# Kernel tuning notes

Hardware: AMD Instinct MI355X
Metric: run time of the kernel (lower is better)

The kernel has to match this reference:

```python
import jax, jax.numpy as jnp
import numpy as np

EPS = 1e-5
NUM_HEADS = 4

# Spiking neuron: single-timestep LIF with threshold 1.0 (Heaviside forward,
# ATan surrogate gradient as in snntorch's default spike_grad).
@jax.custom_vjp
def spike(v):
    return (v >= 1.0).astype(v.dtype)

def _spike_fwd(v):
    return spike(v), v

def _spike_bwd(v, g):
    u = v - 1.0
    return (g / (1.0 + (jnp.pi * u) ** 2),)

spike.defvjp(_spike_fwd, _spike_bwd)

def layernorm(x, g, b):
    mu = jnp.mean(x, axis=-1, keepdims=True)
    var = jnp.var(x, axis=-1, keepdims=True)
    return (x - mu) * jax.lax.rsqrt(var + EPS) * g + b

def batchnorm(x, g, b):
    # BatchNorm1d applied on (B, C, N) == per-channel stats over (B, N) of (B, N, C)
    mu = jnp.mean(x, axis=(0, 1))
    var = jnp.var(x, axis=(0, 1))
    return (x - mu) * jax.lax.rsqrt(var + EPS) * g + b

def lin_bn_spike(x, w, g, b):
    # Linear (no bias) -> BatchNorm1d -> spiking neuron
    return spike(batchnorm(jnp.einsum('bnc,oc->bno', x, w), g, b))


def setup_inputs() -> dict:
    key = jax.random.key(0)
    ks = jax.random.split(key, 8)
    B, N, C = 8, 2048, 256
    Hid = 1024  # int(256 * 4.0)
    s = 0.02
    d = {
        'x': jax.random.normal(ks[0], (B, N, C), jnp.float32),
        'ln1_g': jnp.ones((C,), jnp.float32), 'ln1_b': jnp.zeros((C,), jnp.float32),
        'wq': jax.random.normal(ks[1], (C, C), jnp.float32) * s,
        'q_g': jnp.ones((C,), jnp.float32), 'q_b': jnp.zeros((C,), jnp.float32),
        'wk': jax.random.normal(ks[2], (C, C), jnp.float32) * s,
        'k_g': jnp.ones((C,), jnp.float32), 'k_b': jnp.zeros((C,), jnp.float32),
        'wv': jax.random.normal(ks[3], (C, C), jnp.float32) * s,
        'v_g': jnp.ones((C,), jnp.float32), 'v_b': jnp.zeros((C,), jnp.float32),
        'wo': jax.random.normal(ks[4], (C, C), jnp.float32) * s,
        'ln2_g': jnp.ones((C,), jnp.float32), 'ln2_b': jnp.zeros((C,), jnp.float32),
        'w1': jax.random.normal(ks[5], (Hid, C), jnp.float32) * s,
        'bn1_g': jnp.ones((Hid,), jnp.float32), 'bn1_b': jnp.zeros((Hid,), jnp.float32),
        'w2': jax.random.normal(ks[6], (C, Hid), jnp.float32) * s,
        'bn2_g': jnp.ones((C,), jnp.float32), 'bn2_b': jnp.zeros((C,), jnp.float32),
    }
    return d


def reference(x, ln1_g, ln1_b, wq, q_g, q_b, wk, k_g, k_b, wv, v_g, v_b, wo,
              ln2_g, ln2_b, w1, bn1_g, bn1_b, w2, bn2_g, bn2_b):
    B, N, C = x.shape
    H = NUM_HEADS
    D = C // H
    scale = D ** (-0.5)

    # --- Spiking self-attention on norm1(x) ---
    h = layernorm(x, ln1_g, ln1_b)
    q = lin_bn_spike(h, wq, q_g, q_b)
    k = lin_bn_spike(h, wk, k_g, k_b)
    v = lin_bn_spike(h, wv, v_g, v_b)
    qh = q.reshape(B, N, H, D).transpose(0, 2, 1, 3)
    kh = k.reshape(B, N, H, D).transpose(0, 2, 1, 3)
    vh = v.reshape(B, N, H, D).transpose(0, 2, 1, 3)
    attn = jnp.einsum('bhnd,bhmd->bhnm', qh, kh) * scale  # no softmax
    o = jnp.einsum('bhnm,bhmd->bhnd', attn, vh)
    o = o.transpose(0, 2, 1, 3).reshape(B, N, C)
    x = x + jnp.einsum('bnc,oc->bno', o, wo)

    # --- Spiking MLP on norm2(x) (dropout=0.0) ---
    h = layernorm(x, ln2_g, ln2_b)
    m = lin_bn_spike(h, w1, bn1_g, bn1_b)
    m = lin_bn_spike(m, w2, bn2_g, bn2_b)
    return x + m
```

## Files before the change

kernel.cpp:

```cpp
#include <hip/hip_runtime.h>
#include <cstddef>
#include <cstdint>

#define RR 16384
#define CC 256
#define NN 2048

typedef __attribute__((ext_vector_type(8))) _Float16 h8;
typedef __attribute__((ext_vector_type(4))) float float4v;
typedef unsigned short u16;

__device__ inline float h2f(u16 u) {
  return (float)__builtin_bit_cast(_Float16, u);
}
__device__ inline u16 f2h(float f) {
  return __builtin_bit_cast(u16, (_Float16)f);
}

__global__ __launch_bounds__(256) void ln_split(const float* __restrict__ x,
    const float* __restrict__ g, const float* __restrict__ b,
    u16* __restrict__ out) {
  const int wave = threadIdx.x >> 6, lane = threadIdx.x & 63;
  const int row = (blockIdx.x << 2) + wave;
  const float4 v = ((const float4*)(x + (size_t)row * CC))[lane];
  float s1 = v.x + v.y + v.z + v.w;
  float s2 = v.x * v.x + v.y * v.y + v.z * v.z + v.w * v.w;
#pragma unroll
  for (int o = 32; o > 0; o >>= 1) {
    s1 += __shfl_xor(s1, o);
    s2 += __shfl_xor(s2, o);
  }
  const float mu = s1 * (1.0f / CC);
  const float var = s2 * (1.0f / CC) - mu * mu;
  const float rs = 1.0f / sqrtf(var + 1e-5f);
  const float4 gg = ((const float4*)g)[lane];
  const float4 bb = ((const float4*)b)[lane];
  float o4[4];
  o4[0] = (v.x - mu) * rs * gg.x + bb.x;
  o4[1] = (v.y - mu) * rs * gg.y + bb.y;
  o4[2] = (v.z - mu) * rs * gg.z + bb.z;
  o4[3] = (v.w - mu) * rs * gg.w + bb.w;
  ushort4 hi, lo;
  hi.x = f2h(o4[0]); lo.x = f2h(o4[0] - h2f(hi.x));
  hi.y = f2h(o4[1]); lo.y = f2h(o4[1] - h2f(hi.y));
  hi.z = f2h(o4[2]); lo.z = f2h(o4[2] - h2f(hi.z));
  hi.w = f2h(o4[3]); lo.w = f2h(o4[3] - h2f(hi.w));
  *(ushort4*)(out + (size_t)row * 512 + (lane << 2)) = hi;
  *(ushort4*)(out + (size_t)row * 512 + 256 + (lane << 2)) = lo;
}

__global__ __launch_bounds__(256) void split_all(const float* __restrict__ wq,
    const float* __restrict__ wk, const float* __restrict__ wv,
    const float* __restrict__ wo, const float* __restrict__ w1,
    const float* __restrict__ w2, u16* __restrict__ Wqkv,
    u16* __restrict__ wo2, u16* __restrict__ w12, u16* __restrict__ w22) {
  const int bid = blockIdx.x;
  if (bid < 768) {
    const float* W = (bid < 256) ? wq : (bid < 512) ? wk : wv;
    const int rowoff = (bid >> 8) << 8;
    const int li = (bid & 255) * 256 + threadIdx.x;
    const int o = li >> 8, k = li & 255;
    const float w = W[li];
    const u16 h1 = f2h(w);
    const u16 h2 = f2h(w - h2f(h1));
    u16* base = Wqkv + (size_t)(o + rowoff) * 768;
    base[k] = h1; base[256 + k] = h1; base[512 + k] = h2;
  } else if (bid < 1024) {
    const int li = (bid - 768) * 256 + threadIdx.x;
    const int o = li >> 8, k = li & 255;
    const float w = wo[li];
    const u16 h1 = f2h(w);
    const u16 h2 = f2h(w - h2f(h1));
    u16* base = wo2 + (size_t)o * 512;
    base[k] = h1; base[256 + k] = h2;
  } else if (bid < 2048) {
    const int li = (bid - 1024) * 256 + threadIdx.x;
    w12[li] = f2h(w1[li]);
  } else {
    const int li = (bid - 2048) * 256 + threadIdx.x;
    w22[li] = f2h(w2[li]);
  }
}

template <int BM, int BN, int WM, int WN, int STATS, int MINW, int OUTF16>
__global__ __launch_bounds__(512, MINW) void gemm_sp(
    const u16* __restrict__ A, int AW,
    const u16* __restrict__ W2, int K2,
    const float* __restrict__ resid, void* __restrict__ Yv, int O,
    float* __restrict__ p1, float* __restrict__ p2) {
  constexpr int FM = BM / (WM * 16);
  constexpr int FN = BN / (WN * 16);
  constexpr int LA = BM / 64;
  constexpr int LB = BN / 64;
  constexpr int NL = LA + LB;
  static_assert(WM * WN == 8, "8 waves");
  static_assert(NL == 3 || NL == 4 || NL == 5 || NL == 7 || NL == 8,
                "vmcnt literal");
  __shared__ __align__(16) u16 As[2][BM * 64];
  __shared__ __align__(16) u16 Bs[2][BN * 64];
  const int tid = threadIdx.x;
  const int lane = tid & 63, wid = tid >> 6;
  const int wr = wid / WN, wc = wid % WN;
  const int gx = gridDim.x;
  const int lid = blockIdx.y * gx + blockIdx.x;
  const int chunk = (gx * gridDim.y) >> 3;
  const int nid = (lid & 7) * chunk + (lid >> 3);
  const int bx = nid % gx, by = nid / gx;
  const int r0 = by * BM, o0 = bx * BN;
  const int lrow = tid >> 3;
  const int lce = ((tid & 7) ^ ((tid >> 3) & 7)) << 3;

  auto STAGE = [&](int buf, int kAs, int k0s) {
#pragma unroll
    for (int i = 0; i < LA; ++i) {
      const u16* srcA = A + (size_t)(r0 + i * 64 + lrow) * AW + kAs + lce;
      __builtin_amdgcn_global_load_lds(
          (const __attribute__((address_space(1))) void*)srcA,
          (__attribute__((address_space(3))) void*)&As[buf][(i * 64 + wid * 8) * 64],
          16, 0, 0);
    }
#pragma unroll
    for (int i = 0; i < LB; ++i) {
      const u16* srcB = W2 + (size_t)(o0 + i * 64 + lrow) * K2 + k0s + lce;
      __builtin_amdgcn_global_load_lds(
          (const __attribute__((address_space(1))) void*)srcB,
          (__attribute__((address_space(3))) void*)&Bs[buf][(i * 64 + wid * 8) * 64],
          16, 0, 0);
    }
  };

  float4v acc[FM][FN] = {};
  STAGE(0, 0, 0);
  int kA = 0, cur = 0;
  for (int k0 = 0; k0 < K2; k0 += 64) {
    const int kAn = (kA + 64) & (AW - 1);
    if (k0 + 64 < K2) {
      STAGE(cur ^ 1, kAn, k0 + 64);
      if constexpr (NL == 3)
        asm volatile("s_waitcnt vmcnt(3)\n\ts_barrier" ::: "memory");
      else if constexpr (NL == 4)
        asm volatile("s_waitcnt vmcnt(4)\n\ts_barrier" ::: "memory");
      else if constexpr (NL == 5)
        asm volatile("s_waitcnt vmcnt(5)\n\ts_barrier" ::: "memory");
      else if constexpr (NL == 7)
        asm volatile("s_waitcnt vmcnt(7)\n\ts_barrier" ::: "memory");
      else
        asm volatile("s_waitcnt vmcnt(8)\n\ts_barrier" ::: "memory");
    } else {
      asm volatile("s_waitcnt vmcnt(0)\n\ts_barrier" ::: "memory");
    }
#pragma unroll
    for (int kk = 0; kk < 2; ++kk) {
      h8 a[FM], b[FN];
      const int ch0 = (kk << 2) + (lane >> 4);
      const int chs = ch0 ^ (lane & 7);
#pragma unroll
      for (int m = 0; m < FM; ++m) {
        const int R = wr * (FM * 16) + m * 16 + (lane & 15);
        a[m] = *(const h8*)&As[cur][R * 64 + chs * 8];
      }
#pragma unroll
      for (int n = 0; n < FN; ++n) {
        const int Rb = wc * (FN * 16) + n * 16 + (lane & 15);
        b[n] = *(const h8*)&Bs[cur][Rb * 64 + chs * 8];
      }
#pragma unroll
      for (int m = 0; m < FM; ++m)
#pragma unroll
        for (int n = 0; n < FN; ++n)
          acc[m][n] = __builtin_amdgcn_mfma_f32_16x16x32_f16(a[m], b[n], acc[m][n], 0, 0, 0);
    }
    asm volatile("s_waitcnt lgkmcnt(0)\n\ts_barrier" ::: "memory");
    kA = kAn; cur ^= 1;
  }
  const int crow = (lane >> 4) << 2, ccol = lane & 15;
#pragma unroll
  for (int m = 0; m < FM; ++m)
#pragma unroll
    for (int n = 0; n < FN; ++n)
#pragma unroll
      for (int j = 0; j < 4; ++j) {
        const size_t idx =
            (size_t)(r0 + wr * (FM * 16) + (m << 4) + crow + j) * O +
            o0 + wc * (FN * 16) + (n << 4) + ccol;
        float v = acc[m][n][j];
        if constexpr (OUTF16) {
          ((u16*)Yv)[idx] = f2h(v);
        } else {
          if (resid) v += resid[idx];
          ((float*)Yv)[idx] = v;
        }
      }
  if (STATS) {
    float s1[FN], s2[FN];
#pragma unroll
    for (int n = 0; n < FN; ++n) {
      s1[n] = 0.f; s2[n] = 0.f;
#pragma unroll
      for (int m = 0; m < FM; ++m)
#pragma unroll
        for (int j = 0; j < 4; ++j) {
          const float v = acc[m][n][j];
          s1[n] += v; s2[n] += v * v;
        }
    }
#pragma unroll
    for (int n = 0; n < FN; ++n) {
      s1[n] += __shfl_xor(s1[n], 16); s1[n] += __shfl_xor(s1[n], 32);
      s2[n] += __shfl_xor(s2[n], 16); s2[n] += __shfl_xor(s2[n], 32);
    }
    float* sb = (float*)As;
    __syncthreads();
    if (lane < 16) {
#pragma unroll
      for (int n = 0; n < FN; ++n) {
        const int cl = wc * (FN * 16) + n * 16 + lane;
        sb[wr * BN + cl] = s1[n];
        sb[WM * BN + wr * BN + cl] = s2[n];
      }
    }
    __syncthreads();
    if (tid < BN) {
      float a = 0.f, b = 0.f;
#pragma unroll
      for (int w = 0; w < WM; ++w) {
        a += sb[w * BN + tid];
        b += sb[WM * BN + w * BN + tid];
      }
      p1[(size_t)by * O + o0 + tid] = a;
      p2[(size_t)by * O + o0 + tid] = b;
    }
  }
}

__global__ __launch_bounds__(256) void bn_stats2(const float* __restrict__ p1,
    const float* __restrict__ p2, float* __restrict__ mu,
    float* __restrict__ rinv, int O, int npanels) {
  const int c0 = blockIdx.x << 6;
  const int c = threadIdx.x & 63;
  const int jg = threadIdx.x >> 6;
  float s1 = 0.f, s2 = 0.f;
#pragma unroll 4
  for (int j = jg; j < npanels; j += 4) {
    s1 += p1[(size_t)j * O + c0 + c];
    s2 += p2[(size_t)j * O + c0 + c];
  }
  __shared__ float sb[8][64];
  sb[jg][c] = s1;
  sb[4 + jg][c] = s2;
  __syncthreads();
  if (threadIdx.x < 64) {
    const float a = ((sb[0][c] + sb[1][c]) + (sb[2][c] + sb[3][c]));
    const float b = ((sb[4][c] + sb[5][c]) + (sb[6][c] + sb[7][c]));
    const float m = a * (1.0f / 16384.f);
    const float v = b * (1.0f / 16384.f) - m * m;
    mu[c0 + c] = m;
    rinv[c0 + c] = 1.0f / sqrtf(v + 1e-5f);
  }
}

__global__ __launch_bounds__(256) void bn_spike_h16(const u16* __restrict__ Y,
    const float* __restrict__ mu, const float* __restrict__ rinv,
    const float* __restrict__ g, const float* __restrict__ b,
    u16* __restrict__ S, int O) {
  const int i = blockIdx.x * 256 + threadIdx.x;
  const int c = (i << 2) & (O - 1);
  const ushort4 yh = ((const ushort4*)Y)[i];
  const float4 m4 = *(const float4*)(mu + c);
  const float4 r4 = *(const float4*)(rinv + c);
  const float4 g4 = *(const float4*)(g + c);
  const float4 b4 = *(const float4*)(b + c);
  ushort4 s;
  s.x = ((h2f(yh.x) - m4.x) * r4.x * g4.x + b4.x >= 1.0f) ? (u16)0x3C00 : (u16)0;
  s.y = ((h2f(yh.y) - m4.y) * r4.y * g4.y + b4.y >= 1.0f) ? (u16)0x3C00 : (u16)0;
  s.z = ((h2f(yh.z) - m4.z) * r4.z * g4.z + b4.z >= 1.0f) ? (u16)0x3C00 : (u16)0;
  s.w = ((h2f(yh.w) - m4.w) * r4.w * g4.w + b4.w >= 1.0f) ? (u16)0x3C00 : (u16)0;
  ((ushort4*)S)[i] = s;
}

__global__ __launch_bounds__(256) void bn_spike_add(const float* __restrict__ Y,
    const float* __restrict__ mu, const float* __restrict__ rinv,
    const float* __restrict__ g, const float* __restrict__ b,
    float* __restrict__ addOut, int O) {
  const int i = blockIdx.x * 256 + threadIdx.x;
  const int c = (i << 2) & (O - 1);
  const float4 y = ((const float4*)Y)[i];
  const float4 m4 = *(const float4*)(mu + c);
  const float4 r4 = *(const float4*)(rinv + c);
  const float4 g4 = *(const float4*)(g + c);
  const float4 b4 = *(const float4*)(b + c);
  float4 o4 = ((const float4*)addOut)[i];
  o4.x += ((y.x - m4.x) * r4.x * g4.x + b4.x >= 1.0f) ? 1.0f : 0.0f;
  o4.y += ((y.y - m4.y) * r4.y * g4.y + b4.y >= 1.0f) ? 1.0f : 0.0f;
  o4.z += ((y.z - m4.z) * r4.z * g4.z + b4.z >= 1.0f) ? 1.0f : 0.0f;
  o4.w += ((y.w - m4.w) * r4.w * g4.w + b4.w >= 1.0f) ? 1.0f : 0.0f;
  ((float4*)addOut)[i] = o4;
}

__global__ __launch_bounds__(256) void attn_kv(const float* __restrict__ Yq,
    const float* __restrict__ mu, const float* __restrict__ rinv,
    const float* __restrict__ kg, const float* __restrict__ kb,
    const float* __restrict__ vg, const float* __restrict__ vb,
    float* __restrict__ Mpart) {
  const int bh = blockIdx.x, sp = blockIdx.y;
  const int b = bh >> 2, h = bh & 3;
  const int t = threadIdx.x;
  const int gq = t >> 6, e = t & 63;
  __shared__ float ks[16][64], vs[16][64];
  float acc[16] = {};
  const int lrow = t >> 4, lf = (t & 15) << 2;
  const int c = (h << 6) + lf;
  const int ck = 256 + c, cv = 512 + c;
  const float4 kmu = *(const float4*)(mu + ck);
  const float4 krv = *(const float4*)(rinv + ck);
  const float4 kg4 = *(const float4*)(kg + c);
  const float4 kb4 = *(const float4*)(kb + c);
  const float4 vmu = *(const float4*)(mu + cv);
  const float4 vrv = *(const float4*)(rinv + cv);
  const float4 vg4 = *(const float4*)(vg + c);
  const float4 vb4 = *(const float4*)(vb + c);
  for (int n0 = sp * 128; n0 < sp * 128 + 128; n0 += 16) {
    const size_t rowb = (size_t)(b * NN + n0 + lrow) * 768;
    const float4 kq = *(const float4*)(Yq + rowb + ck);
    const float4 vq = *(const float4*)(Yq + rowb + cv);
    __syncthreads();
    ks[lrow][lf + 0] = ((kq.x - kmu.x) * krv.x * kg4.x + kb4.x >= 1.0f) ? 1.f : 0.f;
    ks[lrow][lf + 1] = ((kq.y - kmu.y) * krv.y * kg4.y + kb4.y >= 1.0f) ? 1.f : 0.f;
    ks[lrow][lf + 2] = ((kq.z - kmu.z) * krv.z * kg4.z + kb4.z >= 1.0f) ? 1.f : 0.f;
    ks[lrow][lf + 3] = ((kq.w - kmu.w) * krv.w * kg4.w + kb4.w >= 1.0f) ? 1.f : 0.f;
    vs[lrow][lf + 0] = ((vq.x - vmu.x) * vrv.x * vg4.x + vb4.x >= 1.0f) ? 1.f : 0.f;
    vs[lrow][lf + 1] = ((vq.y - vmu.y) * vrv.y * vg4.y + vb4.y >= 1.0f) ? 1.f : 0.f;
    vs[lrow][lf + 2] = ((vq.z - vmu.z) * vrv.z * vg4.z + vb4.z >= 1.0f) ? 1.f : 0.f;
    vs[lrow][lf + 3] = ((vq.w - vmu.w) * vrv.w * vg4.w + vb4.w >= 1.0f) ? 1.f : 0.f;
    __syncthreads();
#pragma unroll
    for (int nn = 0; nn < 16; ++nn) {
      const float vv = vs[nn][e];
#pragma unroll
      for (int i = 0; i < 16; ++i) acc[i] += ks[nn][(gq << 4) + i] * vv;
    }
  }
  float* mp = Mpart + ((size_t)bh * 16 + sp) * 4096;
#pragma unroll
  for (int i = 0; i < 16; ++i) mp[((gq << 4) + i) * 64 + e] = acc[i];
}

__global__ __launch_bounds__(256) void attn_kv_reduce(
    const float* __restrict__ Mpart, float* __restrict__ M) {
  const int i = blockIdx.x * 256 + threadIdx.x;
  const int bh = i >> 12, j = i & 4095;
  float s = 0.f;
#pragma unroll
  for (int sp = 0; sp < 16; ++sp)
    s += Mpart[((size_t)bh * 16 + sp) * 4096 + j];
  M[i] = s;
}

__global__ __launch_bounds__(256) void attn_qm(const float* __restrict__ Yq,
    const float* __restrict__ mu, const float* __restrict__ rinv,
    const float* __restrict__ qg, const float* __restrict__ qb,
    const float* __restrict__ M, u16* __restrict__ O2) {
  const int h = blockIdx.x;
  const int r0 = blockIdx.y << 6;
  const int b = blockIdx.y >> 5;
  const int t = threadIdx.x;
  const int e = t & 63, rg = t >> 6;
  __shared__ float Ms[64][64];
  __shared__ float qs[64][64];
  const float* Mb = M + ((size_t)(b * 4 + h) << 12);
  for (int i = t; i < 4096; i += 256) ((float*)Ms)[i] = Mb[i];
  const int c = (h << 6) + e;
  const float qmu = mu[c], qrv = rinv[c], qgg = qg[c], qbb = qb[c];
  for (int rl = rg; rl < 64; rl += 4) {
    const float y = Yq[(size_t)(r0 + rl) * 768 + c];
    qs[rl][e] = ((y - qmu) * qrv * qgg + qbb >= 1.0f) ? 1.f : 0.f;
  }
  __syncthreads();
  for (int rl = rg; rl < 64; rl += 4) {
    float acc = 0.f;
#pragma unroll
    for (int d = 0; d < 64; ++d) acc += qs[rl][d] * Ms[d][e];
    const float o = 0.125f * acc;
    const u16 hi = f2h(o);
    const u16 lo = f2h(o - h2f(hi));
    O2[(size_t)(r0 + rl) * 512 + (h << 6) + e] = hi;
    O2[(size_t)(r0 + rl) * 512 + 256 + (h << 6) + e] = lo;
  }
}

extern "C" void kernel_launch(void* const* d_in, const int* in_sizes, int n_in,
                              void* d_out, int out_size, void* d_ws,
                              size_t ws_size, hipStream_t stream) {
  const float* x    = (const float*)d_in[0];
  const float* ln1g = (const float*)d_in[1];
  const float* ln1b = (const float*)d_in[2];
  const float* wq   = (const float*)d_in[3];
  const float* qg   = (const float*)d_in[4];
  const float* qb   = (const float*)d_in[5];
  const float* wk   = (const float*)d_in[6];
  const float* kg   = (const float*)d_in[7];
  const float* kb   = (const float*)d_in[8];
  const float* wv   = (const float*)d_in[9];
  const float* vg   = (const float*)d_in[10];
  const float* vb   = (const float*)d_in[11];
  const float* wo   = (const float*)d_in[12];
  const float* ln2g = (const float*)d_in[13];
  const float* ln2b = (const float*)d_in[14];
  const float* w1   = (const float*)d_in[15];
  const float* b1g  = (const float*)d_in[16];
  const float* b1b  = (const float*)d_in[17];
  const float* w2   = (const float*)d_in[18];
  const float* b2g  = (const float*)d_in[19];
  const float* b2b  = (const float*)d_in[20];
  float* out = (float*)d_out;
  char* ws = (char*)d_ws;
  const size_t MB = 1u << 20;
  u16*   h1s   = (u16*)(ws);
  float* Yq    = (float*)(ws + 16 * MB);
  float* Mpart = (float*)(ws + 88 * MB);
  float* Mful  = (float*)(ws + 96 * MB);
  u16*   o2    = (u16*)(ws);
  u16*   h2s   = (u16*)(ws + 16 * MB);
  u16*   Ym16  = (u16*)(ws + 32 * MB);
  float* Ym    = (float*)(ws + 32 * MB);
  u16*   m1    = (u16*)(ws + 97 * MB);
  u16*   Wqkv  = (u16*)(ws + 129 * MB);
  u16*   wo2   = (u16*)(ws + 131 * MB);
  u16*   w12   = (u16*)(ws + 132 * MB);
  u16*   w22   = (u16*)(ws + 134 * MB);
  float* p1    = (float*)(ws + 135 * MB);
  float* p2    = (float*)(ws + 136 * MB);
  float* mu    = (float*)(ws + 137 * MB);
  float* rinv  = (float*)(ws + 137 * MB + 32768);

  const dim3 blk(256);
  const dim3 blk512(512);

  split_all<<<3072, blk, 0, stream>>>(wq, wk, wv, wo, w1, w2, Wqkv, wo2, w12, w22);

  ln_split<<<RR / 4, blk, 0, stream>>>(x, ln1g, ln1b, h1s);

  gemm_sp<128, 192, 2, 4, 1, 4, 0><<<dim3(4, 128), blk512, 0, stream>>>(
      h1s, 512, Wqkv, 768, nullptr, Yq, 768, p1, p2);

  bn_stats2<<<12, blk, 0, stream>>>(p1, p2, mu, rinv, 768, 128);

  attn_kv<<<dim3(32, 16), blk, 0, stream>>>(Yq, mu, rinv, kg, kb, vg, vb, Mpart);
  attn_kv_reduce<<<512, blk, 0, stream>>>(Mpart, Mful);
  attn_qm<<<dim3(4, RR / 64), blk, 0, stream>>>(Yq, mu, rinv, qg, qb, Mful, o2);

  gemm_sp<64, 128, 2, 4, 0, 4, 0><<<dim3(2, 256), blk512, 0, stream>>>(
      o2, 512, wo2, 512, x, out, 256, nullptr, nullptr);

  ln_split<<<RR / 4, blk, 0, stream>>>(out, ln2g, ln2b, h2s);

  gemm_sp<128, 128, 2, 4, 1, 4, 1><<<dim3(8, 128), blk512, 0, stream>>>(
      h2s, 512, w12, 256, nullptr, Ym16, 1024, p1, p2);
  bn_stats2<<<16, blk, 0, stream>>>(p1, p2, mu, rinv, 1024, 128);
  bn_spike_h16<<<16384, blk, 0, stream>>>(Ym16, mu, rinv, b1g, b1b, m1, 1024);

  gemm_sp<64, 128, 2, 4, 1, 4, 0><<<dim3(2, 256), blk512, 0, stream>>>(
      m1, 1024, w22, 1024, nullptr, Ym, 256, p1, p2);
  bn_stats2<<<4, blk, 0, stream>>>(p1, p2, mu, rinv, 256, 256);
  bn_spike_add<<<4096, blk, 0, stream>>>(Ym, mu, rinv, b2g, b2b, out, 256);
}
```

Baseline: 178.0 us.

## Fuse LayerNorm2 into output projection GEMM and drop split-fp16 precision

The output projection GEMM now covers full 256-column rows per block, stages its fp32 results in shared memory and computes LayerNorm2 in the epilogue, which removes the separate ln_split launch and one fp32 reread of the residual. The wo weights and attention output are no longer split into hi/lo fp16 pairs, which halves that GEMM's K dimension. The last MLP GEMM also writes fp16 instead of fp32 before the BN-spike-add step. These cuts cost precision: the residual path and the BN2 pre-activations lose bits, which can flip spikes near the threshold, and the wider tile gives the projection GEMM fewer blocks.

```diff
diff --git a/kernel.cpp b/kernel.cpp
--- a/kernel.cpp
+++ b/kernel.cpp
@@ -67,12 +67,7 @@
     base[k] = h1; base[256 + k] = h1; base[512 + k] = h2;
   } else if (bid < 1024) {
     const int li = (bid - 768) * 256 + threadIdx.x;
-    const int o = li >> 8, k = li & 255;
-    const float w = wo[li];
-    const u16 h1 = f2h(w);
-    const u16 h2 = f2h(w - h2f(h1));
-    u16* base = wo2 + (size_t)o * 512;
-    base[k] = h1; base[256 + k] = h2;
+    wo2[li] = f2h(wo[li]);
   } else if (bid < 2048) {
     const int li = (bid - 1024) * 256 + threadIdx.x;
     w12[li] = f2h(w1[li]);
@@ -82,12 +77,15 @@
   }
 }
 
-template <int BM, int BN, int WM, int WN, int STATS, int MINW, int OUTF16>
+template <int BM, int BN, int WM, int WN, int STATS, int MINW, int OUTF16,
+          int LNFUSE>
 __global__ __launch_bounds__(512, MINW) void gemm_sp(
     const u16* __restrict__ A, int AW,
     const u16* __restrict__ W2, int K2,
     const float* __restrict__ resid, void* __restrict__ Yv, int O,
-    float* __restrict__ p1, float* __restrict__ p2) {
+    float* __restrict__ p1, float* __restrict__ p2,
+    const float* __restrict__ lng, const float* __restrict__ lnb,
+    u16* __restrict__ h2out) {
   constexpr int FM = BM / (WM * 16);
   constexpr int FN = BN / (WN * 16);
   constexpr int LA = BM / 64;
@@ -96,6 +94,7 @@
   static_assert(WM * WN == 8, "8 waves");
   static_assert(NL == 3 || NL == 4 || NL == 5 || NL == 7 || NL == 8,
                 "vmcnt literal");
+  static_assert(!LNFUSE || (BM == 64 && BN == 256), "LNFUSE tile");
   __shared__ __align__(16) u16 As[2][BM * 64];
   __shared__ __align__(16) u16 Bs[2][BN * 64];
   const int tid = threadIdx.x;
@@ -174,15 +173,16 @@
     kA = kAn; cur ^= 1;
   }
   const int crow = (lane >> 4) << 2, ccol = lane & 15;
+  float* ft = (float*)Bs;
 #pragma unroll
   for (int m = 0; m < FM; ++m)
 #pragma unroll
     for (int n = 0; n < FN; ++n)
 #pragma unroll
       for (int j = 0; j < 4; ++j) {
-        const size_t idx =
-            (size_t)(r0 + wr * (FM * 16) + (m << 4) + crow + j) * O +
-            o0 + wc * (FN * 16) + (n << 4) + ccol;
+        const int lr = wr * (FM * 16) + (m << 4) + crow + j;
+        const int lc = wc * (FN * 16) + (n << 4) + ccol;
+        const size_t idx = (size_t)(r0 + lr) * O + o0 + lc;
         float v = acc[m][n][j];
         if constexpr (OUTF16) {
           ((u16*)Yv)[idx] = f2h(v);
@@ -190,7 +190,35 @@
           if (resid) v += resid[idx];
           ((float*)Yv)[idx] = v;
         }
-      }
+        if constexpr (LNFUSE) ft[lr * 256 + lc] = v;
+      }
+  if constexpr (LNFUSE) {
+    __syncthreads();
+    const int rr0 = wid << 3;
+    const float4 gg = ((const float4*)lng)[lane];
+    const float4 bb = ((const float4*)lnb)[lane];
+#pragma unroll
+    for (int rr = 0; rr < 8; ++rr) {
+      const int r = rr0 + rr;
+      const float4 v = ((const float4*)ft)[r * 64 + lane];
+      float s1 = v.x + v.y + v.z + v.w;
+      float s2 = v.x * v.x + v.y * v.y + v.z * v.z + v.w * v.w;
+#pragma unroll
+      for (int o = 32; o > 0; o >>= 1) {
+        s1 += __shfl_xor(s1, o);
+        s2 += __shfl_xor(s2, o);
+      }
+      const float mu = s1 * (1.0f / CC);
+      const float var = s2 * (1.0f / CC) - mu * mu;
+      const float rs = 1.0f / sqrtf(var + 1e-5f);
+      ushort4 hh;
+      hh.x = f2h((v.x - mu) * rs * gg.x + bb.x);
+      hh.y = f2h((v.y - mu) * rs * gg.y + bb.y);
+      hh.z = f2h((v.z - mu) * rs * gg.z + bb.z);
+      hh.w = f2h((v.w - mu) * rs * gg.w + bb.w);
+      *(ushort4*)(h2out + (size_t)(r0 + r) * 256 + (lane << 2)) = hh;
+    }
+  }
   if (STATS) {
     float s1[FN], s2[FN];
 #pragma unroll
@@ -278,22 +306,22 @@
   ((ushort4*)S)[i] = s;
 }
 
-__global__ __launch_bounds__(256) void bn_spike_add(const float* __restrict__ Y,
-    const float* __restrict__ mu, const float* __restrict__ rinv,
-    const float* __restrict__ g, const float* __restrict__ b,
-    float* __restrict__ addOut, int O) {
+__global__ __launch_bounds__(256) void bn_spike_add_h16(
+    const u16* __restrict__ Y, const float* __restrict__ mu,
+    const float* __restrict__ rinv, const float* __restrict__ g,
+    const float* __restrict__ b, float* __restrict__ addOut, int O) {
   const int i = blockIdx.x * 256 + threadIdx.x;
   const int c = (i << 2) & (O - 1);
-  const float4 y = ((const float4*)Y)[i];
+  const ushort4 yh = ((const ushort4*)Y)[i];
   const float4 m4 = *(const float4*)(mu + c);
   const float4 r4 = *(const float4*)(rinv + c);
   const float4 g4 = *(const float4*)(g + c);
   const float4 b4 = *(const float4*)(b + c);
   float4 o4 = ((const float4*)addOut)[i];
-  o4.x += ((y.x - m4.x) * r4.x * g4.x + b4.x >= 1.0f) ? 1.0f : 0.0f;
-  o4.y += ((y.y - m4.y) * r4.y * g4.y + b4.y >= 1.0f) ? 1.0f : 0.0f;
-  o4.z += ((y.z - m4.z) * r4.z * g4.z + b4.z >= 1.0f) ? 1.0f : 0.0f;
-  o4.w += ((y.w - m4.w) * r4.w * g4.w + b4.w >= 1.0f) ? 1.0f : 0.0f;
+  o4.x += ((h2f(yh.x) - m4.x) * r4.x * g4.x + b4.x >= 1.0f) ? 1.0f : 0.0f;
+  o4.y += ((h2f(yh.y) - m4.y) * r4.y * g4.y + b4.y >= 1.0f) ? 1.0f : 0.0f;
+  o4.z += ((h2f(yh.z) - m4.z) * r4.z * g4.z + b4.z >= 1.0f) ? 1.0f : 0.0f;
+  o4.w += ((h2f(yh.w) - m4.w) * r4.w * g4.w + b4.w >= 1.0f) ? 1.0f : 0.0f;
   ((float4*)addOut)[i] = o4;
 }
 
@@ -359,7 +387,7 @@
 __global__ __launch_bounds__(256) void attn_qm(const float* __restrict__ Yq,
     const float* __restrict__ mu, const float* __restrict__ rinv,
     const float* __restrict__ qg, const float* __restrict__ qb,
-    const float* __restrict__ M, u16* __restrict__ O2) {
+    const float* __restrict__ M, u16* __restrict__ O1) {
   const int h = blockIdx.x;
   const int r0 = blockIdx.y << 6;
   const int b = blockIdx.y >> 5;
@@ -380,11 +408,7 @@
     float acc = 0.f;
 #pragma unroll
     for (int d = 0; d < 64; ++d) acc += qs[rl][d] * Ms[d][e];
-    const float o = 0.125f * acc;
-    const u16 hi = f2h(o);
-    const u16 lo = f2h(o - h2f(hi));
-    O2[(size_t)(r0 + rl) * 512 + (h << 6) + e] = hi;
-    O2[(size_t)(r0 + rl) * 512 + 256 + (h << 6) + e] = lo;
+    O1[(size_t)(r0 + rl) * 256 + (h << 6) + e] = f2h(0.125f * acc);
   }
 }
 
@@ -419,10 +443,10 @@
   float* Yq    = (float*)(ws + 16 * MB);
   float* Mpart = (float*)(ws + 88 * MB);
   float* Mful  = (float*)(ws + 96 * MB);
-  u16*   o2    = (u16*)(ws);
-  u16*   h2s   = (u16*)(ws + 16 * MB);
+  u16*   o16   = (u16*)(ws);
+  u16*   h2_16 = (u16*)(ws + 16 * MB);
   u16*   Ym16  = (u16*)(ws + 32 * MB);
-  float* Ym    = (float*)(ws + 32 * MB);
+  u16*   Y2    = (u16*)(ws + 64 * MB);
   u16*   m1    = (u16*)(ws + 97 * MB);
   u16*   Wqkv  = (u16*)(ws + 129 * MB);
   u16*   wo2   = (u16*)(ws + 131 * MB);
@@ -440,27 +464,26 @@
 
   ln_split<<<RR / 4, blk, 0, stream>>>(x, ln1g, ln1b, h1s);
 
-  gemm_sp<128, 192, 2, 4, 1, 4, 0><<<dim3(4, 128), blk512, 0, stream>>>(
-      h1s, 512, Wqkv, 768, nullptr, Yq, 768, p1, p2);
+  gemm_sp<128, 192, 2, 4, 1, 4, 0, 0><<<dim3(4, 128), blk512, 0, stream>>>(
+      h1s, 512, Wqkv, 768, nullptr, Yq, 768, p1, p2, nullptr, nullptr, nullptr);
 
   bn_stats2<<<12, blk, 0, stream>>>(p1, p2, mu, rinv, 768, 128);
 
   attn_kv<<<dim3(32, 16), blk, 0, stream>>>(Yq, mu, rinv, kg, kb, vg, vb, Mpart);
   attn_kv_reduce<<<512, blk, 0, stream>>>(Mpart, Mful);
-  attn_qm<<<dim3(4, RR / 64), blk, 0, stream>>>(Yq, mu, rinv, qg, qb, Mful, o2);
-
-  gemm_sp<64, 128, 2, 4, 0, 4, 0><<<dim3(2, 256), blk512, 0, stream>>>(
-      o2, 512, wo2, 512, x, out, 256, nullptr, nullptr);
-
-  ln_split<<<RR / 4, blk, 0, stream>>>(out, ln2g, ln2b, h2s);
-
-  gemm_sp<128, 128, 2, 4, 1, 4, 1><<<dim3(8, 128), blk512, 0, stream>>>(
-      h2s, 512, w12, 256, nullptr, Ym16, 1024, p1, p2);
+  attn_qm<<<dim3(4, RR / 64), blk, 0, stream>>>(Yq, mu, rinv, qg, qb, Mful, o16);
+
+  gemm_sp<64, 256, 2, 4, 0, 4, 0, 1><<<dim3(1, 256), blk512, 0, stream>>>(
+      o16, 256, wo2, 256, x, out, 256, nullptr, nullptr, ln2g, ln2b, h2_16);
+
+  gemm_sp<128, 128, 2, 4, 1, 4, 1, 0><<<dim3(8, 128), blk512, 0, stream>>>(
+      h2_16, 256, w12, 256, nullptr, Ym16, 1024, p1, p2, nullptr, nullptr,
+      nullptr);
   bn_stats2<<<16, blk, 0, stream>>>(p1, p2, mu, rinv, 1024, 128);
   bn_spike_h16<<<16384, blk, 0, stream>>>(Ym16, mu, rinv, b1g, b1b, m1, 1024);
 
-  gemm_sp<64, 128, 2, 4, 1, 4, 0><<<dim3(2, 256), blk512, 0, stream>>>(
-      m1, 1024, w22, 1024, nullptr, Ym, 256, p1, p2);
+  gemm_sp<64, 128, 2, 4, 1, 4, 1, 0><<<dim3(2, 256), blk512, 0, stream>>>(
+      m1, 1024, w22, 1024, nullptr, Y2, 256, p1, p2, nullptr, nullptr, nullptr);
   bn_stats2<<<4, blk, 0, stream>>>(p1, p2, mu, rinv, 256, 256);
-  bn_spike_add<<<4096, blk, 0, stream>>>(Ym, mu, rinv, b2g, b2b, out, 256);
-}
+  bn_spike_add_h16<<<4096, blk, 0, stream>>>(Y2, mu, rinv, b2g, b2b, out, 256);
+}
```

Result: faster. 172.8 us (-2.9%).
